# Optimization experiments

Hardware: AMD Instinct MI355X
Metric: run time of the kernel (lower is better)

The kernel has to match this reference:

```python
import jax, jax.numpy as jnp
import numpy as np

N = 100_000          # nodes
E = 1_600_000        # directed edges
GENE_DIM = 39
NUM_CLASSES = 5
EPS = 1e-5           # BatchNorm1d eps
DIMS = [(GENE_DIM, 64), (64, 128), (128, 64), (64, 32)]


def setup_inputs() -> dict:
    key = jax.random.key(0)
    ks = jax.random.split(key, 32)
    inp = {
        "x": jax.random.normal(ks[0], (N, GENE_DIM), dtype=jnp.float32),
        "edge_index": jax.random.randint(ks[1], (2, E), 0, N, dtype=jnp.int64),
    }
    ki = 2
    for i, (din, dout) in enumerate(DIMS, start=1):
        scale = 1.0 / np.sqrt(din)
        inp[f"W{i}"] = jax.random.uniform(ks[ki], (din, dout), jnp.float32, -scale, scale); ki += 1
        inp[f"b{i}"] = jnp.zeros((dout,), jnp.float32)
        inp[f"g{i}"] = jnp.ones((dout,), jnp.float32)    # BN gamma
        inp[f"be{i}"] = jnp.zeros((dout,), jnp.float32)  # BN beta
    scale = 1.0 / np.sqrt(32)
    inp["Wc"] = jax.random.uniform(ks[ki], (32, NUM_CLASSES), jnp.float32, -scale, scale)
    inp["bc"] = jnp.zeros((NUM_CLASSES,), jnp.float32)
    return inp


def reference(x, edge_index,
              W1, b1, g1, be1,
              W2, b2, g2, be2,
              W3, b3, g3, be3,
              W4, b4, g4, be4,
              Wc, bc):
    n = x.shape[0]
    # --- self loops + symmetric GCN normalization (shared by all 4 convs) ---
    loop = jnp.arange(n, dtype=edge_index.dtype)
    src = jnp.concatenate([edge_index[0], loop])   # message source (x_j)
    dst = jnp.concatenate([edge_index[1], loop])   # aggregation target
    deg = jax.ops.segment_sum(jnp.ones_like(dst, dtype=x.dtype), dst, num_segments=n)
    dinv = jnp.where(deg > 0, jax.lax.rsqrt(deg), 0.0)
    norm = (dinv[src] * dinv[dst])[:, None]        # [E+n, 1]

    def conv(h, W, b):
        # linear transform, gather from source, normalize, scatter-add at target
        m = (h @ W)[src] * norm
        return jax.ops.segment_sum(m, dst, num_segments=n) + b

    def bn(h, g, be):
        # training-mode BatchNorm1d: biased variance over the node axis
        mu = jnp.mean(h, axis=0)
        var = jnp.mean(jnp.square(h - mu), axis=0)
        return g * (h - mu) * jax.lax.rsqrt(var + EPS) + be

    h = bn(jax.nn.relu(conv(x, W1, b1)), g1, be1)
    h = bn(jax.nn.relu(conv(h, W2, b2)), g2, be2)
    h = bn(jax.nn.relu(conv(h, W3, b3)), g3, be3)
    h = bn(jax.nn.relu(conv(h, W4, b4)), g4, be4)
    out = h @ Wc + bc
    return (out, h)
```

## Files before the change

kernel.cpp:

```cpp
#include <hip/hip_runtime.h>

typedef unsigned int uint;
typedef unsigned short ushort;
typedef __attribute__((ext_vector_type(8))) short bf16x8;
typedef __attribute__((ext_vector_type(4))) float f32x4;
typedef __attribute__((ext_vector_type(4))) uint uintx4;

#define N_NODES 100000
#define N_EDGES 1600000
#define NB_C 256
#define TILE_C ((N_EDGES + NB_C - 1) / NB_C)
#define NB_D ((N_NODES + 511) / 512)
#define MG_GRID ((N_NODES + 63) / 64)
#define AGG_GRID 2048
constexpr float BN_EPS = 1e-5f;

__device__ __forceinline__ float bflo(uint w) { return __uint_as_float(w << 16); }
__device__ __forceinline__ float bfhi(uint w) { return __uint_as_float(w & 0xffff0000u); }
__device__ __forceinline__ ushort f2bf(float x) {
    uint u = __float_as_uint(x);
    uint r = (u + 0x7fffu + ((u >> 16) & 1u)) >> 16;
    return (ushort)r;
}
__device__ __forceinline__ uint pack2(float a, float b) {
    return (uint)f2bf(a) | ((uint)f2bf(b) << 16);
}

__device__ __forceinline__ bool detect_i64(const int* __restrict__ ep)
{
    int lane = threadIdx.x & 63;
    unsigned long long nz = __ballot(ep[2 * lane + 1] != 0);
    return nz == 0ULL;
}

__global__ __launch_bounds__(256) void coarseA_kernel(const int* __restrict__ ep,
                                                      uint* __restrict__ ch)
{
    __shared__ uint lh[256];
    int t = threadIdx.x, blk = blockIdx.x;
    lh[t] = 0;
    bool i64 = detect_i64(ep);
    __syncthreads();
    int start = blk * TILE_C;
    int end = start + TILE_C;
    if (end > N_EDGES) end = N_EDGES;
    for (int e = start + t; e < end; e += 256) {
        int d = i64 ? ep[2 * (N_EDGES + e)] : ep[N_EDGES + e];
        atomicAdd(&lh[d >> 9], 1u);
    }
    __syncthreads();
    ch[t * NB_C + blk] = lh[t];
}

__global__ void scanB_kernel(uint* __restrict__ ch, uint* __restrict__ bucketBase)
{
    __shared__ uint tot[256];
    int t = threadIdx.x;
    uint s = 0;
    for (int i = 0; i < NB_C; i++) s += ch[t * NB_C + i];
    tot[t] = s;
    __syncthreads();
    for (int off = 1; off < 256; off <<= 1) {
        uint add = (t >= off) ? tot[t - off] : 0u;
        __syncthreads();
        tot[t] += add;
        __syncthreads();
    }
    uint base = tot[t] - s;
    bucketBase[t] = base;
    if (t == 255) bucketBase[256] = base + s;
    uint run = base;
    for (int i = 0; i < NB_C; i++) {
        uint c = ch[t * NB_C + i];
        ch[t * NB_C + i] = run;
        run += c;
    }
}

__global__ __launch_bounds__(256) void scatterC_kernel(const int* __restrict__ ep,
                                                       const uint* __restrict__ ch,
                                                       int2* __restrict__ pair)
{
    __shared__ uint loff[256];
    int t = threadIdx.x, blk = blockIdx.x;
    loff[t] = ch[t * NB_C + blk];
    bool i64 = detect_i64(ep);
    __syncthreads();
    int start = blk * TILE_C;
    int end = start + TILE_C;
    if (end > N_EDGES) end = N_EDGES;
    for (int e = start + t; e < end; e += 256) {
        int s, d;
        if (i64) { s = ep[2 * e]; d = ep[2 * (N_EDGES + e)]; }
        else     { s = ep[e];     d = ep[N_EDGES + e]; }
        uint pos = atomicAdd(&loff[d >> 9], 1u);
        pair[pos] = make_int2(s, d);
    }
}

__global__ __launch_bounds__(256) void bucketD_kernel(const int2* __restrict__ pair,
                                                      const uint* __restrict__ bucketBase,
                                                      int* __restrict__ rowptr,
                                                      float* __restrict__ dinv,
                                                      int* __restrict__ colidx)
{
    __shared__ uint cnt[512], offp[512], s2[256];
    int bin = blockIdx.x, t = threadIdx.x;
    cnt[t] = 0; cnt[t + 256] = 0;
    __syncthreads();
    uint lo = bucketBase[bin], hi = bucketBase[bin + 1];
    for (uint p = lo + t; p < hi; p += 256)
        atomicAdd(&cnt[pair[p].y & 511], 1u);
    __syncthreads();
    uint a = cnt[2 * t], b = cnt[2 * t + 1];
    s2[t] = a + b;
    __syncthreads();
    for (int off = 1; off < 256; off <<= 1) {
        uint add = (t >= off) ? s2[t - off] : 0u;
        __syncthreads();
        s2[t] += add;
        __syncthreads();
    }
    uint excl = s2[t] - (a + b);
    offp[2 * t] = excl;
    offp[2 * t + 1] = excl + a;
    __syncthreads();
    for (int k = t; k < 512; k += 256) {
        int d = bin * 512 + k;
        if (d < N_NODES) {
            rowptr[d] = (int)(lo + offp[k]);
            dinv[d] = rsqrtf((float)(cnt[k] + 1));
        }
    }
    if (bin == 0 && t == 0) rowptr[N_NODES] = N_EDGES;
    __syncthreads();
    for (uint p = lo + t; p < hi; p += 256) {
        int2 pr = pair[p];
        uint pos = lo + atomicAdd(&offp[pr.y & 511], 1u);
        colidx[pos] = pr.x;
    }
}

__global__ __launch_bounds__(256) void xscale_kernel(const float* __restrict__ x,
                                                     const float* __restrict__ dinv,
                                                     uint* __restrict__ xs)
{
    int idx = blockIdx.x * 256 + threadIdx.x;
    if (idx >= N_NODES * 32) return;
    int i = idx >> 5;
    int u = idx & 31;
    int c0 = 2 * u, c1 = 2 * u + 1;
    float di = dinv[i];
    float v0 = (c0 < 39) ? x[i * 39 + c0] * di : 0.f;
    float v1 = (c1 < 39) ? x[i * 39 + c1] * di : ((c1 == 39) ? di : 0.f);
    xs[idx] = pack2(v0, v1);
}

__global__ void foldpack_kernel(const float* __restrict__ W, const float* __restrict__ s,
                                const float* __restrict__ u, ushort* __restrict__ Wfrag,
                                float* __restrict__ vB, int din, int dout, int K)
{
    int CT = dout >> 4, KT = K >> 5;
    int nf = KT * CT;
    int b = blockIdx.x;
    if (b < nf) {
        int kt = b / CT, ct = b - kt * CT;
        for (int q = threadIdx.x; q < 512; q += 256) {
            int j = q & 7, lane = q >> 3;
            int k = kt * 32 + (lane >> 4) * 8 + j;
            int c = ct * 16 + (lane & 15);
            float v = 0.f;
            if (k < din) {
                float sv = s ? s[k] : 1.f;
                v = sv * W[k * dout + c];
            }
            Wfrag[(size_t)b * 512 + q] = f2bf(v);
        }
    } else {
        int c = threadIdx.x;
        if (u && c < dout) {
            float acc = 0.f;
            for (int k = 0; k < din; k++) acc += u[k] * W[k * dout + c];
            vB[c] = acc;
        }
    }
}

template <int D, int MODE, int WRSUM>
__global__ __launch_bounds__(256) void agg_kernel(
    const ushort* __restrict__ table, const int* __restrict__ rowptr,
    const int* __restrict__ colidx, const float* __restrict__ dinv,
    const float* __restrict__ bias,
    ushort* __restrict__ outB, float* __restrict__ rowsumP,
    float* __restrict__ Psum, float* __restrict__ Psq)
{
    constexpr int LPE = D / 8;
    constexpr int S = 64 / LPE;
    int tid = threadIdx.x;
    int lane = tid & 63, wid = tid >> 6;
    int seg = lane & (LPE - 1);
    int slot = lane / LPE;
    const ushort* segbase = table + seg * 8;

    float bv[8];
    if constexpr (MODE == 1) {
        float4 b0 = *(const float4*)&bias[seg * 8];
        float4 b1 = *(const float4*)&bias[seg * 8 + 4];
        bv[0] = b0.x; bv[1] = b0.y; bv[2] = b0.z; bv[3] = b0.w;
        bv[4] = b1.x; bv[5] = b1.y; bv[6] = b1.z; bv[7] = b1.w;
    }
    float lsum[8] = {}, lsq[8] = {};

    for (int i = blockIdx.x * 4 + wid; i < N_NODES; i += gridDim.x * 4) {
        int iu = __builtin_amdgcn_readfirstlane(i);
        int s0 = rowptr[iu], e0 = rowptr[iu + 1];
        float acc[8] = {};
        if (slot == 0) {
            const uintx4 w = *(const uintx4*)(segbase + (size_t)iu * D);
            acc[0] = bflo(w.x); acc[1] = bfhi(w.x);
            acc[2] = bflo(w.y); acc[3] = bfhi(w.y);
            acc[4] = bflo(w.z); acc[5] = bfhi(w.z);
            acc[6] = bflo(w.w); acc[7] = bfhi(w.w);
        }
        for (int eb = s0; eb < e0; eb += 2 * S) {
            int e1 = eb + slot, e2 = eb + S + slot;
            uintx4 w1 = {0u, 0u, 0u, 0u}, w2 = {0u, 0u, 0u, 0u};
            if (e1 < e0) {
                int j = colidx[e1];
                w1 = *(const uintx4*)(segbase + (size_t)j * D);
            }
            if (e2 < e0) {
                int j = colidx[e2];
                w2 = *(const uintx4*)(segbase + (size_t)j * D);
            }
            acc[0] += bflo(w1.x) + bflo(w2.x);
            acc[1] += bfhi(w1.x) + bfhi(w2.x);
            acc[2] += bflo(w1.y) + bflo(w2.y);
            acc[3] += bfhi(w1.y) + bfhi(w2.y);
            acc[4] += bflo(w1.z) + bflo(w2.z);
            acc[5] += bfhi(w1.z) + bfhi(w2.z);
            acc[6] += bflo(w1.w) + bflo(w2.w);
            acc[7] += bfhi(w1.w) + bfhi(w2.w);
        }
#pragma unroll
        for (int m = LPE; m < 64; m <<= 1) {
#pragma unroll
            for (int v = 0; v < 8; v++) acc[v] += __shfl_xor(acc[v], m);
        }
        if (slot == 0) {
            float di = dinv[iu];
            if constexpr (MODE == 0) {
                uintx4 pk;
                pk.x = pack2(di * acc[0], di * acc[1]);
                pk.y = pack2(di * acc[2], di * acc[3]);
                pk.z = pack2(di * acc[4], di * acc[5]);
                pk.w = pack2(di * acc[6], di * acc[7]);
                *(uintx4*)(outB + (size_t)iu * D + seg * 8) = pk;
                if constexpr (WRSUM) {
                    if (seg == 4) rowsumP[iu] = di * acc[7];
                }
            } else {
                float t[8];
#pragma unroll
                for (int v = 0; v < 8; v++) {
                    t[v] = fmaxf(fmaf(di, acc[v], bv[v]), 0.f);
                    lsum[v] += t[v];
                    lsq[v] += t[v] * t[v];
                }
                uintx4 pk;
                pk.x = pack2(t[0], t[1]); pk.y = pack2(t[2], t[3]);
                pk.z = pack2(t[4], t[5]); pk.w = pack2(t[6], t[7]);
                *(uintx4*)(outB + (size_t)iu * D + seg * 8) = pk;
            }
        }
    }

    if constexpr (MODE == 1) {
        __shared__ float ssum[D], ssq[D];
        for (int c = tid; c < D; c += 256) { ssum[c] = 0.f; ssq[c] = 0.f; }
        __syncthreads();
        if (slot == 0) {
#pragma unroll
            for (int v = 0; v < 8; v++) {
                atomicAdd(&ssum[seg * 8 + v], lsum[v]);
                atomicAdd(&ssq[seg * 8 + v], lsq[v]);
            }
        }
        __syncthreads();
        for (int c = tid; c < D; c += 256) {
            Psum[(size_t)c * gridDim.x + blockIdx.x] = ssum[c];
            Psq[(size_t)c * gridDim.x + blockIdx.x] = ssq[c];
        }
    }
}

template <int K, int DOUT, int MODE>
__global__ __launch_bounds__(256) void mgemm_kernel(
    const ushort* __restrict__ A, const ushort* __restrict__ Wfrag,
    const float* __restrict__ bias, const float* __restrict__ bias2,
    const float* __restrict__ rowsumP, const float* __restrict__ dinv,
    ushort* __restrict__ outB, float* __restrict__ Psum, float* __restrict__ Psq)
{
    constexpr int KT = K / 32, CT = DOUT / 16;
    int tid = threadIdx.x;
    int lane = tid & 63, wid = tid >> 6;
    int r0 = blockIdx.x * 64 + wid * 16;
    int arow = r0 + (lane & 15);
    if (arow >= N_NODES) arow = N_NODES - 1;
    const ushort* aptr = A + (size_t)arow * K + (lane >> 4) * 8;

    f32x4 acc[CT];
#pragma unroll
    for (int ct = 0; ct < CT; ct++) acc[ct] = (f32x4){0.f, 0.f, 0.f, 0.f};

#pragma unroll
    for (int kt = 0; kt < KT; kt++) {
        bf16x8 af = *(const bf16x8*)(aptr + kt * 32);
        const ushort* wp = Wfrag + ((size_t)(kt * CT) * 64 + lane) * 8;
#pragma unroll
        for (int ct = 0; ct < CT; ct++) {
            bf16x8 bfr = *(const bf16x8*)(wp + (size_t)ct * 64 * 8);
            acc[ct] = __builtin_amdgcn_mfma_f32_16x16x32_bf16(af, bfr, acc[ct], 0, 0, 0);
        }
    }

    int colbase = lane & 15;
    int rgrp = lane >> 4;
    int rows[4]; bool rok[4];
    float rP[4], rD[4];
#pragma unroll
    for (int i = 0; i < 4; i++) {
        int r = r0 + rgrp * 4 + i;
        rows[i] = r;
        rok[i] = (r < N_NODES);
        int rc = rok[i] ? r : 0;
        if constexpr (MODE == 1) rP[i] = rowsumP[rc];
        else rD[i] = dinv[rc];
    }

    __shared__ float ssum[DOUT], ssq[DOUT];
    if constexpr (MODE <= 1) {
        for (int c = tid; c < DOUT; c += 256) { ssum[c] = 0.f; ssq[c] = 0.f; }
        __syncthreads();
    }

#pragma unroll
    for (int ct = 0; ct < CT; ct++) {
        int col = ct * 16 + colbase;
        float b = bias[col];
        float b2 = 0.f;
        if constexpr (MODE == 1) b2 = bias2[col];
        float cs = 0.f, cq = 0.f;
#pragma unroll
        for (int i = 0; i < 4; i++) {
            float v = acc[ct][i] + b;
            if constexpr (MODE == 1) v = fmaf(rP[i], b2, v);
            if constexpr (MODE <= 1) v = fmaxf(v, 0.f);
            float w = (MODE == 1) ? v : rD[i] * v;
            if (rok[i]) {
                outB[(size_t)rows[i] * DOUT + col] = f2bf(w);
                if constexpr (MODE <= 1) { cs += v; cq += v * v; }
            }
        }
        if constexpr (MODE <= 1) {
            cs += __shfl_xor(cs, 16); cs += __shfl_xor(cs, 32);
            cq += __shfl_xor(cq, 16); cq += __shfl_xor(cq, 32);
            if (rgrp == 0) {
                atomicAdd(&ssum[col], cs);
                atomicAdd(&ssq[col], cq);
            }
        }
    }
    if constexpr (MODE <= 1) {
        __syncthreads();
        for (int c = tid; c < DOUT; c += 256) {
            Psum[(size_t)c * gridDim.x + blockIdx.x] = ssum[c];
            Psq[(size_t)c * gridDim.x + blockIdx.x] = ssq[c];
        }
    }
}

__global__ __launch_bounds__(256) void reduce_bn_kernel(
    const float* __restrict__ Psum, const float* __restrict__ Psq, int nb,
    const float* __restrict__ g, const float* __restrict__ be,
    float* __restrict__ sOut, float* __restrict__ uOut)
{
    int c = blockIdx.x, t = threadIdx.x;
    float s = 0.f, q = 0.f;
    for (int i = t; i < nb; i += 256) {
        s += Psum[(size_t)c * nb + i];
        q += Psq[(size_t)c * nb + i];
    }
    __shared__ float rs[256], rq[256];
    rs[t] = s; rq[t] = q;
    __syncthreads();
    for (int off = 128; off > 0; off >>= 1) {
        if (t < off) { rs[t] += rs[t + off]; rq[t] += rq[t + off]; }
        __syncthreads();
    }
    if (t == 0) {
        float mu = rs[0] * (1.0f / N_NODES);
        float var = rq[0] * (1.0f / N_NODES) - mu * mu;
        float sv = g[c] * rsqrtf(var + BN_EPS);
        sOut[c] = sv;
        uOut[c] = be[c] - mu * sv;
    }
}

__global__ __launch_bounds__(256) void final_kernel(
    const ushort* __restrict__ t4, const float* __restrict__ sArr,
    const float* __restrict__ uArr, const float* __restrict__ Wc,
    const float* __restrict__ bc, float* __restrict__ out_logits,
    float* __restrict__ out_h)
{
    __shared__ float sc[32], sh2[32], Wcs[160], bcs[5];
    int t = threadIdx.x;
    if (t < 32) { sc[t] = sArr[t]; sh2[t] = uArr[t]; }
    if (t < 160) Wcs[t] = Wc[t];
    if (t < 5) bcs[t] = bc[t];
    __syncthreads();
    int i = blockIdx.x * blockDim.x + t;
    if (i >= N_NODES) return;
    float hv[32];
    const uint* tp = (const uint*)(t4 + (size_t)i * 32);
#pragma unroll
    for (int q = 0; q < 4; q++) {
        uintx4 w = *(const uintx4*)(tp + q * 4);
        int f0 = q * 8;
        hv[f0 + 0] = fmaf(sc[f0 + 0], bflo(w.x), sh2[f0 + 0]);
        hv[f0 + 1] = fmaf(sc[f0 + 1], bfhi(w.x), sh2[f0 + 1]);
        hv[f0 + 2] = fmaf(sc[f0 + 2], bflo(w.y), sh2[f0 + 2]);
        hv[f0 + 3] = fmaf(sc[f0 + 3], bfhi(w.y), sh2[f0 + 3]);
        hv[f0 + 4] = fmaf(sc[f0 + 4], bflo(w.z), sh2[f0 + 4]);
        hv[f0 + 5] = fmaf(sc[f0 + 5], bfhi(w.z), sh2[f0 + 5]);
        hv[f0 + 6] = fmaf(sc[f0 + 6], bflo(w.w), sh2[f0 + 6]);
        hv[f0 + 7] = fmaf(sc[f0 + 7], bfhi(w.w), sh2[f0 + 7]);
    }
#pragma unroll
    for (int f0 = 0; f0 < 32; f0 += 4) {
        float4 v = {hv[f0], hv[f0 + 1], hv[f0 + 2], hv[f0 + 3]};
        *(float4*)&out_h[(size_t)i * 32 + f0] = v;
    }
    float o[5];
#pragma unroll
    for (int c = 0; c < 5; c++) o[c] = bcs[c];
#pragma unroll
    for (int f = 0; f < 32; f++) {
        float hvf = hv[f];
#pragma unroll
        for (int c = 0; c < 5; c++) o[c] = fmaf(hvf, Wcs[f * 5 + c], o[c]);
    }
#pragma unroll
    for (int c = 0; c < 5; c++) out_logits[(size_t)i * 5 + c] = o[c];
}

extern "C" void kernel_launch(void* const* d_in, const int* in_sizes, int n_in,
                              void* d_out, int out_size, void* d_ws, size_t ws_size,
                              hipStream_t stream)
{
    const float* x = (const float*)d_in[0];
    const int* ei = (const int*)d_in[1];
    const float* W1 = (const float*)d_in[2];
    const float* b1 = (const float*)d_in[3];
    const float* g1 = (const float*)d_in[4];
    const float* be1 = (const float*)d_in[5];
    const float* W2 = (const float*)d_in[6];
    const float* b2 = (const float*)d_in[7];
    const float* g2 = (const float*)d_in[8];
    const float* be2 = (const float*)d_in[9];
    const float* W3 = (const float*)d_in[10];
    const float* b3 = (const float*)d_in[11];
    const float* g3 = (const float*)d_in[12];
    const float* be3 = (const float*)d_in[13];
    const float* W4 = (const float*)d_in[14];
    const float* b4 = (const float*)d_in[15];
    const float* g4 = (const float*)d_in[16];
    const float* be4 = (const float*)d_in[17];
    const float* Wc = (const float*)d_in[18];
    const float* bc = (const float*)d_in[19];

    char* ws = (char*)d_ws;
    size_t off = 0;
    auto alloc = [&](size_t bytes) -> void* {
        void* p = ws + off;
        off += (bytes + 255) & ~(size_t)255;
        return p;
    };
    uint* ch = (uint*)alloc(65536 * 4);
    uint* bucketBase = (uint*)alloc(257 * 4);
    int2* pair = (int2*)alloc((size_t)N_EDGES * 8);
    int* rowptr = (int*)alloc((size_t)(N_NODES + 1) * 4);
    float* dinv = (float*)alloc((size_t)N_NODES * 4);
    int* colidx = (int*)alloc((size_t)N_EDGES * 4);
    float* rowsumP = (float*)alloc((size_t)N_NODES * 4);
    uint* xs = (uint*)alloc((size_t)N_NODES * 32 * 4);
    ushort* Wfrag = (ushort*)alloc(32768);
    float* vB = (float*)alloc(128 * 4);
    float* sArr = (float*)alloc(128 * 4);
    float* uArr = (float*)alloc(128 * 4);
    float* Psum = (float*)alloc((size_t)128 * 2048 * 4);
    float* Psq = (float*)alloc((size_t)128 * 2048 * 4);
    ushort* P = (ushort*)alloc((size_t)N_NODES * 64 * 2);
    ushort* Q = (ushort*)alloc((size_t)N_NODES * 64 * 2);
    ushort* R = (ushort*)alloc((size_t)N_NODES * 128 * 2);
    if (off > ws_size) return;

    coarseA_kernel<<<NB_C, 256, 0, stream>>>(ei, ch);
    scanB_kernel<<<1, 256, 0, stream>>>(ch, bucketBase);
    scatterC_kernel<<<NB_C, 256, 0, stream>>>(ei, ch, pair);
    bucketD_kernel<<<NB_D, 256, 0, stream>>>(pair, bucketBase, rowptr, dinv, colidx);

    xscale_kernel<<<(N_NODES * 32 + 255) / 256, 256, 0, stream>>>(x, dinv, xs);
    foldpack_kernel<<<8, 256, 0, stream>>>(W1, nullptr, nullptr, Wfrag, nullptr, 39, 64, 64);

    agg_kernel<64, 0, 1><<<AGG_GRID, 256, 0, stream>>>(
        (const ushort*)xs, rowptr, colidx, dinv, nullptr, P, rowsumP, nullptr, nullptr);
    mgemm_kernel<64, 64, 0><<<MG_GRID, 256, 0, stream>>>(
        P, Wfrag, b1, nullptr, nullptr, dinv, Q, Psum, Psq);
    reduce_bn_kernel<<<64, 256, 0, stream>>>(Psum, Psq, MG_GRID, g1, be1, sArr, uArr);
    foldpack_kernel<<<17, 256, 0, stream>>>(W2, sArr, uArr, Wfrag, vB, 64, 128, 64);

    agg_kernel<64, 0, 0><<<AGG_GRID, 256, 0, stream>>>(
        Q, rowptr, colidx, dinv, nullptr, P, nullptr, nullptr, nullptr);
    mgemm_kernel<64, 128, 1><<<MG_GRID, 256, 0, stream>>>(
        P, Wfrag, b2, vB, rowsumP, nullptr, R, Psum, Psq);
    reduce_bn_kernel<<<128, 256, 0, stream>>>(Psum, Psq, MG_GRID, g2, be2, sArr, uArr);
    foldpack_kernel<<<17, 256, 0, stream>>>(W3, sArr, uArr, Wfrag, vB, 128, 64, 128);

    mgemm_kernel<128, 64, 2><<<MG_GRID, 256, 0, stream>>>(
        R, Wfrag, vB, nullptr, nullptr, dinv, P, nullptr, nullptr);
    agg_kernel<64, 1, 0><<<AGG_GRID, 256, 0, stream>>>(
        P, rowptr, colidx, dinv, b3, Q, nullptr, Psum, Psq);
    reduce_bn_kernel<<<64, 256, 0, stream>>>(Psum, Psq, AGG_GRID, g3, be3, sArr, uArr);
    foldpack_kernel<<<5, 256, 0, stream>>>(W4, sArr, uArr, Wfrag, vB, 64, 32, 64);

    mgemm_kernel<64, 32, 2><<<MG_GRID, 256, 0, stream>>>(
        Q, Wfrag, vB, nullptr, nullptr, dinv, P, nullptr, nullptr);
    agg_kernel<32, 1, 0><<<AGG_GRID, 256, 0, stream>>>(
        P, rowptr, colidx, dinv, b4, R, nullptr, Psum, Psq);
    reduce_bn_kernel<<<32, 256, 0, stream>>>(Psum, Psq, AGG_GRID, g4, be4, sArr, uArr);

    float* out_logits = (float*)d_out;
    float* out_h = (float*)d_out + (size_t)N_NODES * 5;
    final_kernel<<<(N_NODES + 255) / 256, 256, 0, stream>>>(R, sArr, uArr, Wc, bc,
                                                            out_logits, out_h);
}
```

Baseline: 413.5 us.

## Fuse aggregation with MFMA GEMM for first two layers; pack edge pairs

Adds a fused kernel that gathers neighbor rows for a 64-node tile into shared memory and then runs the bf16 MFMA GEMM with bias, ReLU and BN partial sums, replacing separate agg and mgemm launches for layers 1 and 2. This removes the round trip of the aggregated intermediate through global memory and one launch per layer. Separately, the edge-bucketing pair buffer is packed into 32 bits (source plus low 9 destination bits), halving its traffic. The fused kernel uses a fixed grid of 64-row tiles with one wave per 16 rows, so load balance across the gather phase may be worse than the grid-strided agg kernel.

```diff
diff --git a/kernel.cpp b/kernel.cpp
--- a/kernel.cpp
+++ b/kernel.cpp
@@ -79,7 +79,7 @@
 
 __global__ __launch_bounds__(256) void scatterC_kernel(const int* __restrict__ ep,
                                                        const uint* __restrict__ ch,
-                                                       int2* __restrict__ pair)
+                                                       uint* __restrict__ pair)
 {
     __shared__ uint loff[256];
     int t = threadIdx.x, blk = blockIdx.x;
@@ -94,11 +94,11 @@
         if (i64) { s = ep[2 * e]; d = ep[2 * (N_EDGES + e)]; }
         else     { s = ep[e];     d = ep[N_EDGES + e]; }
         uint pos = atomicAdd(&loff[d >> 9], 1u);
-        pair[pos] = make_int2(s, d);
-    }
-}
-
-__global__ __launch_bounds__(256) void bucketD_kernel(const int2* __restrict__ pair,
+        pair[pos] = (uint)s | ((uint)(d & 511) << 17);
+    }
+}
+
+__global__ __launch_bounds__(256) void bucketD_kernel(const uint* __restrict__ pair,
                                                       const uint* __restrict__ bucketBase,
                                                       int* __restrict__ rowptr,
                                                       float* __restrict__ dinv,
@@ -110,7 +110,7 @@
     __syncthreads();
     uint lo = bucketBase[bin], hi = bucketBase[bin + 1];
     for (uint p = lo + t; p < hi; p += 256)
-        atomicAdd(&cnt[pair[p].y & 511], 1u);
+        atomicAdd(&cnt[(pair[p] >> 17) & 511], 1u);
     __syncthreads();
     uint a = cnt[2 * t], b = cnt[2 * t + 1];
     s2[t] = a + b;
@@ -135,9 +135,9 @@
     if (bin == 0 && t == 0) rowptr[N_NODES] = N_EDGES;
     __syncthreads();
     for (uint p = lo + t; p < hi; p += 256) {
-        int2 pr = pair[p];
-        uint pos = lo + atomicAdd(&offp[pr.y & 511], 1u);
-        colidx[pos] = pr.x;
+        uint pr = pair[p];
+        uint pos = lo + atomicAdd(&offp[(pr >> 17) & 511], 1u);
+        colidx[pos] = (int)(pr & 0x1FFFFu);
     }
 }
 
@@ -186,6 +186,134 @@
     }
 }
 
+template <int DOUT, int GMODE, int WRSUM>
+__global__ __launch_bounds__(256) void fused_kernel(
+    const ushort* __restrict__ table, const int* __restrict__ rowptr,
+    const int* __restrict__ colidx, const float* __restrict__ dinv,
+    const ushort* __restrict__ Wfrag, const float* __restrict__ bias,
+    const float* __restrict__ vB, float* __restrict__ rowsumP,
+    ushort* __restrict__ outB, float* __restrict__ Psum, float* __restrict__ Psq)
+{
+    constexpr int KT = 2, CT = DOUT / 16;
+    __shared__ ushort atile[64 * 72];
+    int tid = threadIdx.x, lane = tid & 63, wid = tid >> 6;
+    int seg = lane & 7, slot = lane >> 3;
+    const ushort* segbase = table + seg * 8;
+    int r0 = blockIdx.x * 64;
+
+    for (int t = 0; t < 16; ++t) {
+        int row = wid * 16 + t;
+        int i = r0 + row;
+        float acc[8] = {};
+        if (i < N_NODES) {
+            int s0 = rowptr[i], e0 = rowptr[i + 1];
+            if (slot == 0) {
+                const uintx4 w = *(const uintx4*)(segbase + (size_t)i * 64);
+                acc[0] = bflo(w.x); acc[1] = bfhi(w.x);
+                acc[2] = bflo(w.y); acc[3] = bfhi(w.y);
+                acc[4] = bflo(w.z); acc[5] = bfhi(w.z);
+                acc[6] = bflo(w.w); acc[7] = bfhi(w.w);
+            }
+            for (int eb = s0; eb < e0; eb += 16) {
+                int e1 = eb + slot, e2 = eb + 8 + slot;
+                uintx4 w1 = {0u, 0u, 0u, 0u}, w2 = {0u, 0u, 0u, 0u};
+                if (e1 < e0) w1 = *(const uintx4*)(segbase + (size_t)colidx[e1] * 64);
+                if (e2 < e0) w2 = *(const uintx4*)(segbase + (size_t)colidx[e2] * 64);
+                acc[0] += bflo(w1.x) + bflo(w2.x);
+                acc[1] += bfhi(w1.x) + bfhi(w2.x);
+                acc[2] += bflo(w1.y) + bflo(w2.y);
+                acc[3] += bfhi(w1.y) + bfhi(w2.y);
+                acc[4] += bflo(w1.z) + bflo(w2.z);
+                acc[5] += bfhi(w1.z) + bfhi(w2.z);
+                acc[6] += bflo(w1.w) + bflo(w2.w);
+                acc[7] += bfhi(w1.w) + bfhi(w2.w);
+            }
+#pragma unroll
+            for (int m = 8; m < 64; m <<= 1) {
+#pragma unroll
+                for (int v = 0; v < 8; v++) acc[v] += __shfl_xor(acc[v], m);
+            }
+        }
+        if (slot == 0) {
+            float di = (i < N_NODES) ? dinv[i] : 0.f;
+            uintx4 pk;
+            pk.x = pack2(di * acc[0], di * acc[1]);
+            pk.y = pack2(di * acc[2], di * acc[3]);
+            pk.z = pack2(di * acc[4], di * acc[5]);
+            pk.w = pack2(di * acc[6], di * acc[7]);
+            *(uintx4*)&atile[row * 72 + seg * 8] = pk;
+            if constexpr (WRSUM) {
+                if (seg == 4 && i < N_NODES) rowsumP[i] = di * acc[7];
+            }
+        }
+    }
+
+    const ushort* aptr = &atile[(wid * 16 + (lane & 15)) * 72 + (lane >> 4) * 8];
+    f32x4 gacc[CT];
+#pragma unroll
+    for (int ct = 0; ct < CT; ct++) gacc[ct] = (f32x4){0.f, 0.f, 0.f, 0.f};
+#pragma unroll
+    for (int kt = 0; kt < KT; kt++) {
+        bf16x8 af = *(const bf16x8*)(aptr + kt * 32);
+        const ushort* wp = Wfrag + ((size_t)(kt * CT) * 64 + lane) * 8;
+#pragma unroll
+        for (int ct = 0; ct < CT; ct++) {
+            bf16x8 bfr = *(const bf16x8*)(wp + (size_t)ct * 64 * 8);
+            gacc[ct] = __builtin_amdgcn_mfma_f32_16x16x32_bf16(af, bfr, gacc[ct], 0, 0, 0);
+        }
+    }
+
+    int colbase = lane & 15;
+    int rgrp = lane >> 4;
+    int r0w = r0 + wid * 16;
+    int rows[4]; bool rok[4];
+    float rP[4], rD[4];
+#pragma unroll
+    for (int i = 0; i < 4; i++) {
+        int r = r0w + rgrp * 4 + i;
+        rows[i] = r;
+        rok[i] = (r < N_NODES);
+        int rc = rok[i] ? r : 0;
+        if constexpr (GMODE == 1) rP[i] = rowsumP[rc];
+        else rD[i] = dinv[rc];
+    }
+
+    __shared__ float ssum[DOUT], ssq[DOUT];
+    for (int c = tid; c < DOUT; c += 256) { ssum[c] = 0.f; ssq[c] = 0.f; }
+    __syncthreads();
+
+#pragma unroll
+    for (int ct = 0; ct < CT; ct++) {
+        int col = ct * 16 + colbase;
+        float b = bias[col];
+        float b2 = 0.f;
+        if constexpr (GMODE == 1) b2 = vB[col];
+        float cs = 0.f, cq = 0.f;
+#pragma unroll
+        for (int i = 0; i < 4; i++) {
+            float v = gacc[ct][i] + b;
+            if constexpr (GMODE == 1) v = fmaf(rP[i], b2, v);
+            v = fmaxf(v, 0.f);
+            float w = (GMODE == 1) ? v : rD[i] * v;
+            if (rok[i]) {
+                outB[(size_t)rows[i] * DOUT + col] = f2bf(w);
+                cs += v; cq += v * v;
+            }
+        }
+        cs += __shfl_xor(cs, 16); cs += __shfl_xor(cs, 32);
+        cq += __shfl_xor(cq, 16); cq += __shfl_xor(cq, 32);
+        if (rgrp == 0) {
+            atomicAdd(&ssum[col], cs);
+            atomicAdd(&ssq[col], cq);
+        }
+    }
+    __syncthreads();
+    for (int c = tid; c < DOUT; c += 256) {
+        Psum[(size_t)c * gridDim.x + blockIdx.x] = ssum[c];
+        Psq[(size_t)c * gridDim.x + blockIdx.x] = ssq[c];
+    }
+}
+
 template <int D, int MODE, int WRSUM>
 __global__ __launch_bounds__(256) void agg_kernel(
     const ushort* __restrict__ table, const int* __restrict__ rowptr,
@@ -225,14 +353,8 @@
         for (int eb = s0; eb < e0; eb += 2 * S) {
             int e1 = eb + slot, e2 = eb + S + slot;
             uintx4 w1 = {0u, 0u, 0u, 0u}, w2 = {0u, 0u, 0u, 0u};
-            if (e1 < e0) {
-                int j = colidx[e1];
-                w1 = *(const uintx4*)(segbase + (size_t)j * D);
-            }
-            if (e2 < e0) {
-                int j = colidx[e2];
-                w2 = *(const uintx4*)(segbase + (size_t)j * D);
-            }
+            if (e1 < e0) w1 = *(const uintx4*)(segbase + (size_t)colidx[e1] * D);
+            if (e2 < e0) w2 = *(const uintx4*)(segbase + (size_t)colidx[e2] * D);
             acc[0] += bflo(w1.x) + bflo(w2.x);
             acc[1] += bfhi(w1.x) + bfhi(w2.x);
             acc[2] += bflo(w1.y) + bflo(w2.y);
@@ -327,55 +449,25 @@
     int colbase = lane & 15;
     int rgrp = lane >> 4;
     int rows[4]; bool rok[4];
-    float rP[4], rD[4];
+    float rD[4];
 #pragma unroll
     for (int i = 0; i < 4; i++) {
         int r = r0 + rgrp * 4 + i;
         rows[i] = r;
         rok[i] = (r < N_NODES);
         int rc = rok[i] ? r : 0;
-        if constexpr (MODE == 1) rP[i] = rowsumP[rc];
-        else rD[i] = dinv[rc];
-    }
-
-    __shared__ float ssum[DOUT], ssq[DOUT];
-    if constexpr (MODE <= 1) {
-        for (int c = tid; c < DOUT; c += 256) { ssum[c] = 0.f; ssq[c] = 0.f; }
-        __syncthreads();
+        rD[i] = dinv[rc];
     }
 
 #pragma unroll
     for (int ct = 0; ct < CT; ct++) {
         int col = ct * 16 + colbase;
         float b = bias[col];
-        float b2 = 0.f;
-        if constexpr (MODE == 1) b2 = bias2[col];
-        float cs = 0.f, cq = 0.f;
 #pragma unroll
         for (int i = 0; i < 4; i++) {
             float v = acc[ct][i] + b;
-            if constexpr (MODE == 1) v = fmaf(rP[i], b2, v);
-            if constexpr (MODE <= 1) v = fmaxf(v, 0.f);
-            float w = (MODE == 1) ? v : rD[i] * v;
-            if (rok[i]) {
-                outB[(size_t)rows[i] * DOUT + col] = f2bf(w);
-                if constexpr (MODE <= 1) { cs += v; cq += v * v; }
-            }
-        }
-        if constexpr (MODE <= 1) {
-            cs += __shfl_xor(cs, 16); cs += __shfl_xor(cs, 32);
-            cq += __shfl_xor(cq, 16); cq += __shfl_xor(cq, 32);
-            if (rgrp == 0) {
-                atomicAdd(&ssum[col], cs);
-                atomicAdd(&ssq[col], cq);
-            }
-        }
-    }
-    if constexpr (MODE <= 1) {
-        __syncthreads();
-        for (int c = tid; c < DOUT; c += 256) {
-            Psum[(size_t)c * gridDim.x + blockIdx.x] = ssum[c];
-            Psq[(size_t)c * gridDim.x + blockIdx.x] = ssq[c];
+            float w = rD[i] * v;
+            if (rok[i]) outB[(size_t)rows[i] * DOUT + col] = f2bf(w);
         }
     }
 }
@@ -488,7 +580,7 @@
     };
     uint* ch = (uint*)alloc(65536 * 4);
     uint* bucketBase = (uint*)alloc(257 * 4);
-    int2* pair = (int2*)alloc((size_t)N_EDGES * 8);
+    uint* pair = (uint*)alloc((size_t)N_EDGES * 4);
     int* rowptr = (int*)alloc((size_t)(N_NODES + 1) * 4);
     float* dinv = (float*)alloc((size_t)N_NODES * 4);
     int* colidx = (int*)alloc((size_t)N_EDGES * 4);
@@ -513,17 +605,15 @@
     xscale_kernel<<<(N_NODES * 32 + 255) / 256, 256, 0, stream>>>(x, dinv, xs);
     foldpack_kernel<<<8, 256, 0, stream>>>(W1, nullptr, nullptr, Wfrag, nullptr, 39, 64, 64);
 
-    agg_kernel<64, 0, 1><<<AGG_GRID, 256, 0, stream>>>(
-        (const ushort*)xs, rowptr, colidx, dinv, nullptr, P, rowsumP, nullptr, nullptr);
-    mgemm_kernel<64, 64, 0><<<MG_GRID, 256, 0, stream>>>(
-        P, Wfrag, b1, nullptr, nullptr, dinv, Q, Psum, Psq);
+    fused_kernel<64, 0, 1><<<MG_GRID, 256, 0, stream>>>(
+        (const ushort*)xs, rowptr, colidx, dinv, Wfrag, b1, nullptr, rowsumP,
+        Q, Psum, Psq);
     reduce_bn_kernel<<<64, 256, 0, stream>>>(Psum, Psq, MG_GRID, g1, be1, sArr, uArr);
     foldpack_kernel<<<17, 256, 0, stream>>>(W2, sArr, uArr, Wfrag, vB, 64, 128, 64);
 
-    agg_kernel<64, 0, 0><<<AGG_GRID, 256, 0, stream>>>(
-        Q, rowptr, colidx, dinv, nullptr, P, nullptr, nullptr, nullptr);
-    mgemm_kernel<64, 128, 1><<<MG_GRID, 256, 0, stream>>>(
-        P, Wfrag, b2, vB, rowsumP, nullptr, R, Psum, Psq);
+    fused_kernel<128, 1, 0><<<MG_GRID, 256, 0, stream>>>(
+        Q, rowptr, colidx, dinv, Wfrag, b2, vB, rowsumP,
+        R, Psum, Psq);
     reduce_bn_kernel<<<128, 256, 0, stream>>>(Psum, Psq, MG_GRID, g2, be2, sArr, uArr);
     foldpack_kernel<<<17, 256, 0, stream>>>(W3, sArr, uArr, Wfrag, vB, 128, 64, 128);
 
```

New measurement: 479.2 us. 15.9% more time.
